# Performance work log

Measured on AMD Instinct MI355X. Metric: run time of the kernel, lower is better.

The kernel has to match this reference:

```python
import jax, jax.numpy as jnp
import numpy as np

EPS = 1e-6
GAIN = 0.3

def setup_inputs() -> dict:
    key = jax.random.key(0)
    k1, k2 = jax.random.split(key)
    B, C, H, W = 8, 1024, 64, 64
    C_MID = 8
    z = jax.random.normal(k1, (B, C, H, W), dtype=jnp.float32)
    # down conv weight (c_mid, c_in); up weight is its transpose (PCA-ish projector)
    W_down = jax.random.normal(k2, (C_MID, C), dtype=jnp.float32) / np.sqrt(C)
    return {"z": z, "W_down": W_down}

def reference(z, W_down):
    # GroupNorm(1, C, affine=False): normalize over (C,H,W) per sample
    mu = jnp.mean(z, axis=(1, 2, 3), keepdims=True)
    var = jnp.var(z, axis=(1, 2, 3), keepdims=True)
    x = (z - mu) * jax.lax.rsqrt(var + EPS)
    # 1x1 conv down: (B,C,H,W) x (M,C) -> (B,M,H,W)
    y = jnp.einsum('bchw,mc->bmhw', x, W_down)
    # 1x1 conv up with weight = down^T: (B,M,H,W) x (M,C) -> (B,C,H,W)
    r = jnp.einsum('bmhw,mc->bchw', y, W_down)
    return z + GAIN * r
```

## Files before the change

kernel.cpp:

```cpp
#include <hip/hip_runtime.h>
#include <math.h>

#define B    8
#define C    1024
#define M    8
#define HW   4096
#define EPS  1e-6f
#define GAIN 0.3f

#define NT   4
#define NC   8
#define NP   (NT*NC)
#define HWT  (HW/NT)
#define CCH  (C/NC)
#define TPB  256

typedef float floatx4 __attribute__((ext_vector_type(4)));

#define OFF_YZP   0
#define OFF_STATP (OFF_YZP + B*NC*M*HW)
#define OFF_Y     (OFF_STATP + B*NP*2)

__global__ __launch_bounds__(TPB) void k1_partial(const float* __restrict__ z,
                                                  const float* __restrict__ Wd,
                                                  float* __restrict__ ws) {
    int bid = blockIdx.x;
    int nc  = bid % NC;
    int t   = (bid / NC) % NT;
    int b   = bid / (NC * NT);
    int tid = threadIdx.x;
    int hw  = t * HWT + tid * 4;
    int c0  = nc * CCH;

    float4 ym[M];
#pragma unroll
    for (int m = 0; m < M; ++m) ym[m] = make_float4(0.f, 0.f, 0.f, 0.f);
    float su = 0.f, sq = 0.f;

    const float* zp = z + ((size_t)(b * C + c0)) * HW + hw;
#pragma unroll 4
    for (int ci = 0; ci < CCH; ++ci) {
        float4 v = *reinterpret_cast<const float4*>(zp + (size_t)ci * HW);
        su += (v.x + v.y) + (v.z + v.w);
        sq += v.x * v.x + v.y * v.y + v.z * v.z + v.w * v.w;
        int c = c0 + ci;
#pragma unroll
        for (int m = 0; m < M; ++m) {
            float w = Wd[m * C + c];
            ym[m].x += w * v.x;
            ym[m].y += w * v.y;
            ym[m].z += w * v.z;
            ym[m].w += w * v.w;
        }
    }

    float* yzp = ws + OFF_YZP + ((size_t)(b * NC + nc) * M) * HW + hw;
#pragma unroll
    for (int m = 0; m < M; ++m)
        *reinterpret_cast<float4*>(yzp + (size_t)m * HW) = ym[m];

    __shared__ float red[2 * TPB];
    red[tid] = su;
    red[TPB + tid] = sq;
    __syncthreads();
    for (int s = TPB / 2; s > 0; s >>= 1) {
        if (tid < s) {
            red[tid] += red[tid + s];
            red[TPB + tid] += red[TPB + tid + s];
        }
        __syncthreads();
    }
    if (tid == 0) {
        float* st = ws + OFF_STATP + ((size_t)b * NP + t * NC + nc) * 2;
        st[0] = red[0];
        st[1] = red[TPB];
    }
}

__global__ __launch_bounds__(TPB) void k2_reduce_y(const float* __restrict__ Wd,
                                                   float* __restrict__ ws) {
    int bid   = blockIdx.x;
    int b     = bid >> 5;
    int m     = (bid & 31) >> 2;
    int hwblk = bid & 3;
    int tid   = threadIdx.x;
    int wv    = tid >> 6;
    int l     = tid & 63;
    int hw    = hwblk * 1024 + tid * 4;

    __shared__ float sh[3];

    if (wv == 0) {
        float su = 0.f, sq = 0.f;
        if (l < NP) {
            const float* sp = ws + OFF_STATP + ((size_t)b * NP + l) * 2;
            su = sp[0];
            sq = sp[1];
        }
#pragma unroll
        for (int o = 16; o > 0; o >>= 1) {
            su += __shfl_down(su, o);
            sq += __shfl_down(sq, o);
        }
        if (l == 0) {
            const float invN = 1.0f / (float)(C * HW);
            float mu  = su * invN;
            float var = sq * invN - mu * mu;
            sh[0] = mu;
            sh[1] = 1.0f / sqrtf(var + EPS);
        }
    } else if (wv == 1) {
        float sm = 0.f;
#pragma unroll
        for (int k = 0; k < C / 64; ++k) sm += Wd[m * C + k * 64 + l];
#pragma unroll
        for (int o = 32; o > 0; o >>= 1) sm += __shfl_down(sm, o);
        if (l == 0) sh[2] = sm;
    }
    __syncthreads();
    float mu   = sh[0];
    float istd = sh[1];
    float off  = mu * sh[2];

    float4 acc = make_float4(0.f, 0.f, 0.f, 0.f);
    const float* p = ws + OFF_YZP + ((size_t)b * NC * M + m) * HW + hw;
#pragma unroll
    for (int ncp = 0; ncp < NC; ++ncp) {
        float4 v = *reinterpret_cast<const float4*>(p + (size_t)ncp * M * HW);
        acc.x += v.x; acc.y += v.y; acc.z += v.z; acc.w += v.w;
    }
    float4 y;
    y.x = istd * (acc.x - off);
    y.y = istd * (acc.y - off);
    y.z = istd * (acc.z - off);
    y.w = istd * (acc.w - off);
    *reinterpret_cast<float4*>(ws + OFF_Y + ((size_t)b * M + m) * HW + hw) = y;
}

__global__ __launch_bounds__(TPB) void k3_apply(const float* __restrict__ z,
                                                const float* __restrict__ Wd,
                                                const float* __restrict__ ws,
                                                float* __restrict__ out) {
    int bid = blockIdx.x;
    int nc  = bid % NC;
    int t   = (bid / NC) % NT;
    int b   = bid / (NC * NT);
    int tid = threadIdx.x;
    int hw  = t * HWT + tid * 4;
    int c0  = nc * CCH;

    float4 y[M];
    const float* yp = ws + OFF_Y + (size_t)b * M * HW + hw;
#pragma unroll
    for (int m = 0; m < M; ++m)
        y[m] = *reinterpret_cast<const float4*>(yp + (size_t)m * HW);

    const float* zp = z + ((size_t)(b * C + c0)) * HW + hw;
    float* op = out + ((size_t)(b * C + c0)) * HW + hw;
#pragma unroll 4
    for (int ci = 0; ci < CCH; ++ci) {
        float4 v = *reinterpret_cast<const float4*>(zp + (size_t)ci * HW);
        int c = c0 + ci;
        float rx = 0.f, ry = 0.f, rz = 0.f, rw = 0.f;
#pragma unroll
        for (int m = 0; m < M; ++m) {
            float w = Wd[m * C + c];
            rx += w * y[m].x;
            ry += w * y[m].y;
            rz += w * y[m].z;
            rw += w * y[m].w;
        }
        floatx4 o;
        o.x = v.x + GAIN * rx;
        o.y = v.y + GAIN * ry;
        o.z = v.z + GAIN * rz;
        o.w = v.w + GAIN * rw;
        __builtin_nontemporal_store(o, reinterpret_cast<floatx4*>(op + (size_t)ci * HW));
    }
}

extern "C" void kernel_launch(void* const* d_in, const int* in_sizes, int n_in,
                              void* d_out, int out_size, void* d_ws, size_t ws_size,
                              hipStream_t stream) {
    const float* z  = (const float*)d_in[0];
    const float* Wd = (const float*)d_in[1];
    float* out = (float*)d_out;
    float* ws  = (float*)d_ws;

    dim3 blk(TPB);
    k1_partial<<<dim3(B * NT * NC), blk, 0, stream>>>(z, Wd, ws);
    k2_reduce_y<<<dim3(B * M * 4), blk, 0, stream>>>(Wd, ws);
    k3_apply<<<dim3(B * NT * NC), blk, 0, stream>>>(z, Wd, ws, out);
}
```

Before: 72.86 us.

## Split batch into two halves and double channel chunks per launch

Runs the three-kernel pipeline twice, once per half of the batch, so that each half's input (64 MB) is more likely to still be in the last-level cache when the apply kernel re-reads z. Channel chunking doubles from 8 to 16, which keeps the block count per launch the same but doubles the per-chunk partial-y traffic in the reduce kernel. The trade-off is six launches instead of three and less parallelism available within each launch.

```diff
diff --git a/kernel.cpp b/kernel.cpp
--- a/kernel.cpp
+++ b/kernel.cpp
@@ -2,6 +2,7 @@
 #include <math.h>
 
 #define B    8
+#define BH   4
 #define C    1024
 #define M    8
 #define HW   4096
@@ -9,7 +10,7 @@
 #define GAIN 0.3f
 
 #define NT   4
-#define NC   8
+#define NC   16
 #define NP   (NT*NC)
 #define HWT  (HW/NT)
 #define CCH  (C/NC)
@@ -18,16 +19,18 @@
 typedef float floatx4 __attribute__((ext_vector_type(4)));
 
 #define OFF_YZP   0
-#define OFF_STATP (OFF_YZP + B*NC*M*HW)
+#define OFF_STATP (OFF_YZP + BH*NC*M*HW)
 #define OFF_Y     (OFF_STATP + B*NP*2)
 
 __global__ __launch_bounds__(TPB) void k1_partial(const float* __restrict__ z,
                                                   const float* __restrict__ Wd,
-                                                  float* __restrict__ ws) {
+                                                  float* __restrict__ ws,
+                                                  int b0) {
     int bid = blockIdx.x;
     int nc  = bid % NC;
     int t   = (bid / NC) % NT;
-    int b   = bid / (NC * NT);
+    int bl  = bid / (NC * NT);
+    int b   = b0 + bl;
     int tid = threadIdx.x;
     int hw  = t * HWT + tid * 4;
     int c0  = nc * CCH;
@@ -54,7 +57,7 @@
         }
     }
 
-    float* yzp = ws + OFF_YZP + ((size_t)(b * NC + nc) * M) * HW + hw;
+    float* yzp = ws + OFF_YZP + ((size_t)(bl * NC + nc) * M) * HW + hw;
 #pragma unroll
     for (int m = 0; m < M; ++m)
         *reinterpret_cast<float4*>(yzp + (size_t)m * HW) = ym[m];
@@ -78,11 +81,13 @@
 }
 
 __global__ __launch_bounds__(TPB) void k2_reduce_y(const float* __restrict__ Wd,
-                                                   float* __restrict__ ws) {
+                                                   float* __restrict__ ws,
+                                                   int b0) {
     int bid   = blockIdx.x;
-    int b     = bid >> 5;
+    int bl    = bid >> 5;
     int m     = (bid & 31) >> 2;
     int hwblk = bid & 3;
+    int b     = b0 + bl;
     int tid   = threadIdx.x;
     int wv    = tid >> 6;
     int l     = tid & 63;
@@ -91,14 +96,10 @@
     __shared__ float sh[3];
 
     if (wv == 0) {
-        float su = 0.f, sq = 0.f;
-        if (l < NP) {
-            const float* sp = ws + OFF_STATP + ((size_t)b * NP + l) * 2;
-            su = sp[0];
-            sq = sp[1];
-        }
+        const float* sp = ws + OFF_STATP + ((size_t)b * NP + l) * 2;
+        float su = sp[0], sq = sp[1];
 #pragma unroll
-        for (int o = 16; o > 0; o >>= 1) {
+        for (int o = 32; o > 0; o >>= 1) {
             su += __shfl_down(su, o);
             sq += __shfl_down(sq, o);
         }
@@ -123,7 +124,7 @@
     float off  = mu * sh[2];
 
     float4 acc = make_float4(0.f, 0.f, 0.f, 0.f);
-    const float* p = ws + OFF_YZP + ((size_t)b * NC * M + m) * HW + hw;
+    const float* p = ws + OFF_YZP + ((size_t)bl * NC * M + m) * HW + hw;
 #pragma unroll
     for (int ncp = 0; ncp < NC; ++ncp) {
         float4 v = *reinterpret_cast<const float4*>(p + (size_t)ncp * M * HW);
@@ -140,11 +141,12 @@
 __global__ __launch_bounds__(TPB) void k3_apply(const float* __restrict__ z,
                                                 const float* __restrict__ Wd,
                                                 const float* __restrict__ ws,
-                                                float* __restrict__ out) {
+                                                float* __restrict__ out,
+                                                int b0) {
     int bid = blockIdx.x;
     int nc  = bid % NC;
     int t   = (bid / NC) % NT;
-    int b   = bid / (NC * NT);
+    int b   = b0 + bid / (NC * NT);
     int tid = threadIdx.x;
     int hw  = t * HWT + tid * 4;
     int c0  = nc * CCH;
@@ -188,7 +190,10 @@
     float* ws  = (float*)d_ws;
 
     dim3 blk(TPB);
-    k1_partial<<<dim3(B * NT * NC), blk, 0, stream>>>(z, Wd, ws);
-    k2_reduce_y<<<dim3(B * M * 4), blk, 0, stream>>>(Wd, ws);
-    k3_apply<<<dim3(B * NT * NC), blk, 0, stream>>>(z, Wd, ws, out);
+    for (int h = 0; h < 2; ++h) {
+        int b0 = h * BH;
+        k1_partial<<<dim3(BH * NT * NC), blk, 0, stream>>>(z, Wd, ws, b0);
+        k2_reduce_y<<<dim3(BH * M * 4), blk, 0, stream>>>(Wd, ws, b0);
+        k3_apply<<<dim3(BH * NT * NC), blk, 0, stream>>>(z, Wd, ws, out, b0);
+    }
 }
```

Measured after the change: 81.03 us. 1.11x slower.

## Split channel loops across waves and raise block count in partial and apply kernels

Applied to the files above, without the earlier changes.

The partial-projection kernel now splits each block's 128 channels across four waves and combines their partial y sums and statistics in shared memory, quadrupling the grid. The apply kernel uses two channel halves per block with a larger spatial tile, also giving more blocks, and runs blocks in reverse order so recently read z data may still be cached. The aim is better GPU occupancy and latency hiding on a memory-bound pipeline, at the cost of extra LDS traffic and a synchronisation in the first kernel.

```diff
diff --git a/kernel.cpp b/kernel.cpp
--- a/kernel.cpp
+++ b/kernel.cpp
@@ -7,30 +7,39 @@
 #define HW   4096
 #define EPS  1e-6f
 #define GAIN 0.3f
-
-#define NT   4
-#define NC   8
-#define NP   (NT*NC)
-#define HWT  (HW/NT)
-#define CCH  (C/NC)
 #define TPB  256
 
 typedef float floatx4 __attribute__((ext_vector_type(4)));
 
+#define NT1  16
+#define NC1  8
+#define HWT1 256
+#define CCH1 128
+
+#define NT3  8
+#define NC3  16
+#define HWT3 512
+#define CCH3 64
+
 #define OFF_YZP   0
-#define OFF_STATP (OFF_YZP + B*NC*M*HW)
-#define OFF_Y     (OFF_STATP + B*NP*2)
+#define OFF_Y     (OFF_YZP + B*NC1*M*HW)
+#define OFF_STATP (OFF_Y + B*M*HW)
 
 __global__ __launch_bounds__(TPB) void k1_partial(const float* __restrict__ z,
                                                   const float* __restrict__ Wd,
                                                   float* __restrict__ ws) {
-    int bid = blockIdx.x;
-    int nc  = bid % NC;
-    int t   = (bid / NC) % NT;
-    int b   = bid / (NC * NT);
-    int tid = threadIdx.x;
-    int hw  = t * HWT + tid * 4;
-    int c0  = nc * CCH;
+    const int bid = blockIdx.x;
+    const int nc  = bid & 7;
+    const int t   = (bid >> 3) & 15;
+    const int b   = bid >> 7;
+    const int tid = threadIdx.x;
+    const int h   = tid >> 6;
+    const int s   = tid & 63;
+    const int hw  = t * HWT1 + s * 4;
+    const int c0  = nc * CCH1 + h * 32;
+
+    __shared__ __align__(16) float4 scr[3][M][64];
+    __shared__ float sred[2 * TPB];
 
     float4 ym[M];
 #pragma unroll
@@ -39,7 +48,7 @@
 
     const float* zp = z + ((size_t)(b * C + c0)) * HW + hw;
 #pragma unroll 4
-    for (int ci = 0; ci < CCH; ++ci) {
+    for (int ci = 0; ci < 32; ++ci) {
         float4 v = *reinterpret_cast<const float4*>(zp + (size_t)ci * HW);
         su += (v.x + v.y) + (v.z + v.w);
         sq += v.x * v.x + v.y * v.y + v.z * v.z + v.w * v.w;
@@ -47,58 +56,63 @@
 #pragma unroll
         for (int m = 0; m < M; ++m) {
             float w = Wd[m * C + c];
-            ym[m].x += w * v.x;
-            ym[m].y += w * v.y;
-            ym[m].z += w * v.z;
-            ym[m].w += w * v.w;
-        }
-    }
-
-    float* yzp = ws + OFF_YZP + ((size_t)(b * NC + nc) * M) * HW + hw;
-#pragma unroll
-    for (int m = 0; m < M; ++m)
-        *reinterpret_cast<float4*>(yzp + (size_t)m * HW) = ym[m];
-
-    __shared__ float red[2 * TPB];
-    red[tid] = su;
-    red[TPB + tid] = sq;
+            ym[m].x += w * v.x; ym[m].y += w * v.y;
+            ym[m].z += w * v.z; ym[m].w += w * v.w;
+        }
+    }
+
+    if (h > 0) {
+#pragma unroll
+        for (int m = 0; m < M; ++m) scr[h - 1][m][s] = ym[m];
+    }
+    sred[tid] = su;
+    sred[TPB + tid] = sq;
     __syncthreads();
-    for (int s = TPB / 2; s > 0; s >>= 1) {
-        if (tid < s) {
-            red[tid] += red[tid + s];
-            red[TPB + tid] += red[TPB + tid + s];
+    if (h == 0) {
+        float* yzp = ws + OFF_YZP + ((size_t)((b * NC1 + nc) * M)) * HW + hw;
+#pragma unroll
+        for (int m = 0; m < M; ++m) {
+            float4 a = ym[m];
+            float4 p1 = scr[0][m][s], p2 = scr[1][m][s], p3 = scr[2][m][s];
+            a.x += (p1.x + p2.x) + p3.x;
+            a.y += (p1.y + p2.y) + p3.y;
+            a.z += (p1.z + p2.z) + p3.z;
+            a.w += (p1.w + p2.w) + p3.w;
+            *reinterpret_cast<float4*>(yzp + (size_t)m * HW) = a;
+        }
+    }
+    for (int r = TPB / 2; r > 0; r >>= 1) {
+        if (tid < r) {
+            sred[tid] += sred[tid + r];
+            sred[TPB + tid] += sred[TPB + tid + r];
         }
         __syncthreads();
     }
     if (tid == 0) {
-        float* st = ws + OFF_STATP + ((size_t)b * NP + t * NC + nc) * 2;
-        st[0] = red[0];
-        st[1] = red[TPB];
+        ws[OFF_STATP + bid * 2]     = sred[0];
+        ws[OFF_STATP + bid * 2 + 1] = sred[TPB];
     }
 }
 
 __global__ __launch_bounds__(TPB) void k2_reduce_y(const float* __restrict__ Wd,
                                                    float* __restrict__ ws) {
-    int bid   = blockIdx.x;
-    int b     = bid >> 5;
-    int m     = (bid & 31) >> 2;
-    int hwblk = bid & 3;
-    int tid   = threadIdx.x;
-    int wv    = tid >> 6;
-    int l     = tid & 63;
-    int hw    = hwblk * 1024 + tid * 4;
+    const int bid   = blockIdx.x;
+    const int b     = bid >> 5;
+    const int m     = (bid >> 2) & 7;
+    const int hwblk = bid & 3;
+    const int tid   = threadIdx.x;
+    const int wv    = tid >> 6;
+    const int l     = tid & 63;
+    const int hw    = hwblk * 1024 + tid * 4;
 
     __shared__ float sh[3];
 
     if (wv == 0) {
-        float su = 0.f, sq = 0.f;
-        if (l < NP) {
-            const float* sp = ws + OFF_STATP + ((size_t)b * NP + l) * 2;
-            su = sp[0];
-            sq = sp[1];
-        }
-#pragma unroll
-        for (int o = 16; o > 0; o >>= 1) {
+        const float* sp = ws + OFF_STATP + (size_t)(b * 128 + l) * 2;
+        float su = sp[0] + sp[128];
+        float sq = sp[1] + sp[129];
+#pragma unroll
+        for (int o = 32; o > 0; o >>= 1) {
             su += __shfl_down(su, o);
             sq += __shfl_down(sq, o);
         }
@@ -118,15 +132,14 @@
         if (l == 0) sh[2] = sm;
     }
     __syncthreads();
-    float mu   = sh[0];
-    float istd = sh[1];
-    float off  = mu * sh[2];
+    const float istd = sh[1];
+    const float off  = sh[0] * sh[2];
 
     float4 acc = make_float4(0.f, 0.f, 0.f, 0.f);
-    const float* p = ws + OFF_YZP + ((size_t)b * NC * M + m) * HW + hw;
-#pragma unroll
-    for (int ncp = 0; ncp < NC; ++ncp) {
-        float4 v = *reinterpret_cast<const float4*>(p + (size_t)ncp * M * HW);
+    const float* p = ws + OFF_YZP + ((size_t)(b * NC1 * M + m)) * HW + hw;
+#pragma unroll
+    for (int ncp = 0; ncp < NC1; ++ncp) {
+        float4 v = *reinterpret_cast<const float4*>(p + (size_t)(ncp * M) * HW);
         acc.x += v.x; acc.y += v.y; acc.z += v.z; acc.w += v.w;
     }
     float4 y;
@@ -134,47 +147,45 @@
     y.y = istd * (acc.y - off);
     y.z = istd * (acc.z - off);
     y.w = istd * (acc.w - off);
-    *reinterpret_cast<float4*>(ws + OFF_Y + ((size_t)b * M + m) * HW + hw) = y;
+    *reinterpret_cast<float4*>(ws + OFF_Y + ((size_t)(b * M + m)) * HW + hw) = y;
 }
 
 __global__ __launch_bounds__(TPB) void k3_apply(const float* __restrict__ z,
                                                 const float* __restrict__ Wd,
                                                 const float* __restrict__ ws,
                                                 float* __restrict__ out) {
-    int bid = blockIdx.x;
-    int nc  = bid % NC;
-    int t   = (bid / NC) % NT;
-    int b   = bid / (NC * NT);
-    int tid = threadIdx.x;
-    int hw  = t * HWT + tid * 4;
-    int c0  = nc * CCH;
-
-    float4 y[M];
+    const int rbid = (B * NT3 * NC3 - 1) - blockIdx.x;
+    const int nc  = rbid & 15;
+    const int t   = (rbid >> 4) & 7;
+    const int b   = rbid >> 7;
+    const int tid = threadIdx.x;
+    const int h   = tid >> 7;
+    const int s   = tid & 127;
+    const int hw  = t * HWT3 + s * 4;
+    const int c0  = nc * CCH3 + h * 32;
+
+    float4 y4[M];
     const float* yp = ws + OFF_Y + (size_t)b * M * HW + hw;
 #pragma unroll
     for (int m = 0; m < M; ++m)
-        y[m] = *reinterpret_cast<const float4*>(yp + (size_t)m * HW);
+        y4[m] = *reinterpret_cast<const float4*>(yp + (size_t)m * HW);
 
     const float* zp = z + ((size_t)(b * C + c0)) * HW + hw;
     float* op = out + ((size_t)(b * C + c0)) * HW + hw;
 #pragma unroll 4
-    for (int ci = 0; ci < CCH; ++ci) {
+    for (int ci = 0; ci < 32; ++ci) {
         float4 v = *reinterpret_cast<const float4*>(zp + (size_t)ci * HW);
         int c = c0 + ci;
-        float rx = 0.f, ry = 0.f, rz = 0.f, rw = 0.f;
+        float r0 = 0.f, r1 = 0.f, r2 = 0.f, r3 = 0.f;
 #pragma unroll
         for (int m = 0; m < M; ++m) {
             float w = Wd[m * C + c];
-            rx += w * y[m].x;
-            ry += w * y[m].y;
-            rz += w * y[m].z;
-            rw += w * y[m].w;
+            r0 += w * y4[m].x; r1 += w * y4[m].y;
+            r2 += w * y4[m].z; r3 += w * y4[m].w;
         }
         floatx4 o;
-        o.x = v.x + GAIN * rx;
-        o.y = v.y + GAIN * ry;
-        o.z = v.z + GAIN * rz;
-        o.w = v.w + GAIN * rw;
+        o.x = v.x + GAIN * r0; o.y = v.y + GAIN * r1;
+        o.z = v.z + GAIN * r2; o.w = v.w + GAIN * r3;
         __builtin_nontemporal_store(o, reinterpret_cast<floatx4*>(op + (size_t)ci * HW));
     }
 }
@@ -188,7 +199,7 @@
     float* ws  = (float*)d_ws;
 
     dim3 blk(TPB);
-    k1_partial<<<dim3(B * NT * NC), blk, 0, stream>>>(z, Wd, ws);
+    k1_partial<<<dim3(B * NT1 * NC1), blk, 0, stream>>>(z, Wd, ws);
     k2_reduce_y<<<dim3(B * M * 4), blk, 0, stream>>>(Wd, ws);
-    k3_apply<<<dim3(B * NT * NC), blk, 0, stream>>>(z, Wd, ws, out);
-}
+    k3_apply<<<dim3(B * NT3 * NC3), blk, 0, stream>>>(z, Wd, ws, out);
+}
```

Result: no change. 73.67 us (+1.1%).
